# Kernel optimization log

Measured on AMD Instinct MI355X. Metric: run time of the kernel, lower is better.

The kernel has to match this reference:

```python
import jax, jax.numpy as jnp
import numpy as np

B, D, U = 4096, 1024, 1024  # batch, complex input dim, units


def _bias(u):
    # unit_forget_bias: zeros with forget-gate slice (i,f,c,o ordering) set to 1
    return jnp.zeros((4 * u,), jnp.float32).at[u:2 * u].set(1.0)


def setup_inputs() -> dict:
    key = jax.random.key(0)
    ks = jax.random.split(key, 7)
    s = 0.02  # kernel init scale
    return {
        "inputs": jax.random.normal(ks[0], (B, 2 * D), jnp.float32),
        "h_tm1": jax.random.normal(ks[1], (B, 2 * U), jnp.float32),
        "c_tm1": jax.random.normal(ks[2], (B, 2 * U), jnp.float32),
        "real_kernel": s * jax.random.normal(ks[3], (D, 4 * U), jnp.float32),
        "imaginary_kernel": s * jax.random.normal(ks[4], (D, 4 * U), jnp.float32),
        "real_recurrent_kernel": s * jax.random.normal(ks[5], (U, 4 * U), jnp.float32),
        "imaginary_recurrent_kernel": s * jax.random.normal(ks[6], (U, 4 * U), jnp.float32),
        "real_bias": _bias(U),
        "imaginary_bias": _bias(U),
    }


def hard_sigmoid(x):
    # keras hard_sigmoid: clip(0.2*x + 0.5, 0, 1)
    return jnp.clip(0.2 * x + 0.5, 0.0, 1.0)


def reference(inputs, h_tm1, c_tm1, real_kernel, imaginary_kernel,
              real_recurrent_kernel, imaginary_recurrent_kernel,
              real_bias, imaginary_bias):
    d = real_kernel.shape[0]
    u = real_recurrent_kernel.shape[0]
    xr, xi = inputs[:, :d], inputs[:, d:]          # [B,D] real/imag
    hr, hi = h_tm1[:, :u], h_tm1[:, u:]            # [B,U]
    # x @ [[R,-I],[I,R]] == [xr@R + xi@I, xi@R - xr@I]; done once over all 4 gates
    zr = xr @ real_kernel + xi @ imaginary_kernel \
         + hr @ real_recurrent_kernel + hi @ imaginary_recurrent_kernel + real_bias      # [B,4U]
    zi = xi @ real_kernel - xr @ imaginary_kernel \
         + hi @ real_recurrent_kernel - hr @ imaginary_recurrent_kernel + imaginary_bias  # [B,4U]

    def gate(g):  # concatenated real|imag pre-activation for gate g (i,f,c,o)
        s = slice(g * u, (g + 1) * u)
        return jnp.concatenate([zr[:, s], zi[:, s]], axis=-1)  # [B,2U]

    i = hard_sigmoid(gate(0))
    f = hard_sigmoid(gate(1))
    c = f * c_tm1 + i * jnp.tanh(gate(2))
    o = hard_sigmoid(gate(3))
    h = o * jnp.tanh(c)
    return h, c
```

## Files before the change

kernel.cpp:

```cpp
#include <hip/hip_runtime.h>

typedef unsigned short u16;
typedef unsigned int   u32;

typedef __bf16 bf16x8 __attribute__((ext_vector_type(8)));
typedef float  f32x4  __attribute__((ext_vector_type(4)));

typedef const __attribute__((address_space(1))) u32 GAS;
typedef __attribute__((address_space(3))) u32 LAS;

__device__ __forceinline__ u16 f2bf(float f) {
  u32 u = __builtin_bit_cast(u32, f);
  return (u16)((u + 0x7FFFu + ((u >> 16) & 1u)) >> 16);
}

__global__ __launch_bounds__(256) void build_x_k(
    const float* __restrict__ inp, const float* __restrict__ h,
    u16* __restrict__ X3) {
  __shared__ float t[64 * 65];
  const int tid = threadIdx.x;
  const int tx = tid & 15, ty = tid >> 4;
  const int m0 = blockIdx.y * 64, k0 = blockIdx.x * 64;
  const int sel = k0 >> 10;
  const int kc = k0 & 1023;
  const float* s1 = (sel == 0 || sel == 2 || sel == 4) ? inp : h;
  const int c1 = (sel == 2 || sel == 3) ? (1024 + kc) : kc;
  const bool pair = (sel >= 4);
#pragma unroll
  for (int rr = 0; rr < 4; ++rr) {
    const int m = rr * 16 + ty;
    float4 v = *(const float4*)&s1[(size_t)(m0 + m) * 2048 + c1 + tx * 4];
    if (pair) {
      const float4 w = *(const float4*)&s1[(size_t)(m0 + m) * 2048 + c1 + 1024 + tx * 4];
      v.x += w.x; v.y += w.y; v.z += w.z; v.w += w.w;
    }
    t[(tx * 4 + 0) * 65 + m] = v.x;
    t[(tx * 4 + 1) * 65 + m] = v.y;
    t[(tx * 4 + 2) * 65 + m] = v.z;
    t[(tx * 4 + 3) * 65 + m] = v.w;
  }
  __syncthreads();
#pragma unroll
  for (int rep = 0; rep < 2; ++rep) {
    const int cell = rep * 256 + tid;
    const int kblk = cell >> 6, m = cell & 63;
    union { u16 s[8]; uint4 v; } tmp;
#pragma unroll
    for (int i = 0; i < 8; ++i) tmp.s[i] = f2bf(t[(kblk * 8 + i) * 65 + m]);
    *(uint4*)&X3[((size_t)(k0 / 8 + kblk) * 4096 + m0 + m) * 8] = tmp.v;
  }
}

__global__ __launch_bounds__(256) void build_w_k(
    const float* __restrict__ Kr, const float* __restrict__ Ki,
    const float* __restrict__ Rr, const float* __restrict__ Ri,
    u16* __restrict__ W3) {
  __shared__ float t[4 * 1032];
  const int tid = threadIdx.x;
  const int tx = tid & 15, ty = tid >> 4;
  const int jhi = blockIdx.y;
  const int k0 = blockIdx.x * 64;
  const int sel = k0 >> 10;
  const int krow = k0 & 1023;
  const int jbase = jhi * 16;
  const float* sA = (sel == 0) ? Kr : (sel == 1) ? Rr : (sel == 2) ? Ki
                  : (sel == 3) ? Ri : (sel == 4) ? Kr : Rr;
  const float* sB = (sel == 4) ? Ki : (sel == 5) ? Ri : nullptr;
#pragma unroll
  for (int g = 0; g < 4; ++g) {
    const int cs = g * 1024 + jbase + tx;
#pragma unroll
    for (int rr = 0; rr < 4; ++rr) {
      const int k = rr * 16 + ty;
      float v = sA[(size_t)(krow + k) * 4096 + cs];
      if (sel >= 4) v -= sB[(size_t)(krow + k) * 4096 + cs];
      t[g * 1032 + k * 16 + tx] = v;
    }
  }
  __syncthreads();
#pragma unroll
  for (int rep = 0; rep < 2; ++rep) {
    const int cell = rep * 256 + tid;
    const int kblk = cell >> 6, n = cell & 63;
    const int g = n >> 4, jlo = n & 15;
    union { u16 s[8]; uint4 v; } tmp;
#pragma unroll
    for (int i = 0; i < 8; ++i)
      tmp.s[i] = f2bf(t[g * 1032 + (kblk * 8 + i) * 16 + jlo]);
    *(uint4*)&W3[((size_t)(k0 / 8 + kblk) * 4096 + (size_t)jhi * 64 + n) * 8] = tmp.v;
  }
}

#define KT 96

#define SLOT_BODY(ACC)                                                      \
  _Pragma("unroll")                                                         \
  for (int ks = 0; ks < 2; ++ks) {                                          \
    bf16x8 af[4], bfr[4];                                                   \
    _Pragma("unroll")                                                       \
    for (int mf = 0; mf < 4; ++mf)                                          \
      af[mf] = *(const bf16x8*)&buf[aoff + ks * 4096 + mf * 128];           \
    _Pragma("unroll")                                                       \
    for (int nf = 0; nf < 4; ++nf)                                          \
      bfr[nf] = *(const bf16x8*)&buf[boff + ks * 8192 + nf * 128];          \
    __builtin_amdgcn_s_setprio(1);                                          \
    _Pragma("unroll")                                                       \
    for (int mf = 0; mf < 4; ++mf)                                          \
      _Pragma("unroll")                                                     \
      for (int nf = 0; nf < 4; ++nf)                                        \
        ACC[mf][nf] = __builtin_amdgcn_mfma_f32_16x16x32_bf16(              \
            af[mf], bfr[nf], ACC[mf][nf], 0, 0, 0);                         \
    __builtin_amdgcn_s_setprio(0);                                          \
  }

__global__ __launch_bounds__(512, 2) void clstm_gemm_k(
    const u16* __restrict__ X3, const u16* __restrict__ W3,
    const float* __restrict__ cprev, const float* __restrict__ rb,
    const float* __restrict__ ib, float* __restrict__ out) {
  __shared__ __align__(16) u16 lds[3][24576];
  const int tid = threadIdx.x;
  const int lane = tid & 63, wave = tid >> 6;
  const int wr = wave >> 2, wc = wave & 3;
  const int orig = blockIdx.x;
  const int wg = (orig & 7) * 64 + (orig >> 3);
  const int mb = wg & 31, nb = wg >> 5;
  const int m0 = mb * 128, n0 = nb * 256;

  f32x4 a1[4][4] = {}, a2[4][4] = {};

  auto stage = [&](int t, int bi) {
    u16* buf = &lds[bi][0];
    const size_t kb0 = (size_t)t * 8;
#pragma unroll
    for (int i = 0; i < 6; ++i) {
      const int c = wave * 6 + i;
      if (c < 16) {
        const int kblk = c >> 1, half = c & 1;
        const u16* g = X3 + ((kb0 + kblk) * 4096 + (size_t)(m0 + half * 64 + lane)) * 8;
        __builtin_amdgcn_global_load_lds((GAS*)g, (LAS*)&buf[(kblk * 128 + half * 64) * 8],
                                         16, 0, 0);
      } else {
        const int cc = c - 16, kblk = cc >> 2, grp = cc & 3;
        const u16* g = W3 + ((kb0 + kblk) * 4096 + (size_t)(n0 + grp * 64 + lane)) * 8;
        __builtin_amdgcn_global_load_lds((GAS*)g,
                                         (LAS*)&buf[8192 + (kblk * 256 + grp * 64) * 8],
                                         16, 0, 0);
      }
    }
  };

  auto slot_sync = [&](int t, int stb) {
    if (t < KT - 1)
      asm volatile("s_waitcnt vmcnt(6)" ::: "memory");
    else
      asm volatile("s_waitcnt vmcnt(0)" ::: "memory");
    __builtin_amdgcn_s_barrier();
    __builtin_amdgcn_sched_barrier(0);
    if (t + 2 < KT) stage(t + 2, stb);
  };

  const int hi = lane >> 4, lo = lane & 15;
  const int aoff = (hi * 128 + wr * 64 + lo) * 8;
  const int boff = 8192 + (hi * 256 + wc * 64 + lo) * 8;

  stage(0, 0);
  stage(1, 1);
  int cb = 0;

  for (int t = 0; t < 32; ++t) {
    int stb = cb + 2; if (stb >= 3) stb -= 3;
    slot_sync(t, stb);
    const u16* buf = &lds[cb][0];
    SLOT_BODY(a1)
    ++cb; if (cb == 3) cb = 0;
  }
  for (int t = 32; t < 64; ++t) {
    int stb = cb + 2; if (stb >= 3) stb -= 3;
    slot_sync(t, stb);
    const u16* buf = &lds[cb][0];
    SLOT_BODY(a2)
    ++cb; if (cb == 3) cb = 0;
  }
#pragma unroll
  for (int mf = 0; mf < 4; ++mf)
#pragma unroll
    for (int nf = 0; nf < 4; ++nf) {
      const f32x4 t0 = a1[mf][nf];
      a1[mf][nf] = t0 + a2[mf][nf];
      a2[mf][nf] = a2[mf][nf] - t0;
    }
  for (int t = 64; t < KT; ++t) {
    int stb = cb + 2; if (stb >= 3) stb -= 3;
    slot_sync(t, stb);
    const u16* buf = &lds[cb][0];
    SLOT_BODY(a2)
    ++cb; if (cb == 3) cb = 0;
  }

  const int j = (nb * 4 + wc) * 16 + lo;
  float rbias[4], ibias[4];
#pragma unroll
  for (int g = 0; g < 4; ++g) {
    rbias[g] = rb[g * 1024 + j];
    ibias[g] = ib[g * 1024 + j];
  }
#pragma unroll
  for (int mf = 0; mf < 4; ++mf) {
    const int rowb = m0 + wr * 64 + mf * 16 + hi * 4;
#pragma unroll
    for (int r = 0; r < 4; ++r) {
      const size_t row = (size_t)(rowb + r);
      {
        const float z0 = a1[mf][0][r] + rbias[0];
        const float z1 = a1[mf][1][r] + rbias[1];
        const float z2 = a1[mf][2][r] + rbias[2];
        const float z3 = a1[mf][3][r] + rbias[3];
        const float ig = fminf(fmaxf(0.2f * z0 + 0.5f, 0.0f), 1.0f);
        const float fg = fminf(fmaxf(0.2f * z1 + 0.5f, 0.0f), 1.0f);
        const float og = fminf(fmaxf(0.2f * z3 + 0.5f, 0.0f), 1.0f);
        const float cp = cprev[row * 2048 + j];
        const float cn = fg * cp + ig * tanhf(z2);
        const float hn = og * tanhf(cn);
        out[row * 2048 + j] = hn;
        out[(size_t)8388608 + row * 2048 + j] = cn;
      }
      {
        const float z0 = a2[mf][0][r] + ibias[0];
        const float z1 = a2[mf][1][r] + ibias[1];
        const float z2 = a2[mf][2][r] + ibias[2];
        const float z3 = a2[mf][3][r] + ibias[3];
        const float ig = fminf(fmaxf(0.2f * z0 + 0.5f, 0.0f), 1.0f);
        const float fg = fminf(fmaxf(0.2f * z1 + 0.5f, 0.0f), 1.0f);
        const float og = fminf(fmaxf(0.2f * z3 + 0.5f, 0.0f), 1.0f);
        const float cp = cprev[row * 2048 + 1024 + j];
        const float cn = fg * cp + ig * tanhf(z2);
        const float hn = og * tanhf(cn);
        out[row * 2048 + 1024 + j] = hn;
        out[(size_t)8388608 + row * 2048 + 1024 + j] = cn;
      }
    }
  }
}

extern "C" void kernel_launch(void* const* d_in, const int* in_sizes, int n_in,
                              void* d_out, int out_size, void* d_ws, size_t ws_size,
                              hipStream_t stream) {
  const float* inputs = (const float*)d_in[0];
  const float* h_tm1  = (const float*)d_in[1];
  const float* c_tm1  = (const float*)d_in[2];
  const float* Kr     = (const float*)d_in[3];
  const float* Ki     = (const float*)d_in[4];
  const float* Rr     = (const float*)d_in[5];
  const float* Ri     = (const float*)d_in[6];
  const float* rb     = (const float*)d_in[7];
  const float* ib     = (const float*)d_in[8];
  float* out = (float*)d_out;

  u16* X3 = (u16*)d_ws;
  u16* W3 = X3 + (size_t)768 * 4096 * 8;

  build_x_k<<<dim3(96, 64), 256, 0, stream>>>(inputs, h_tm1, X3);
  build_w_k<<<dim3(96, 64), 256, 0, stream>>>(Kr, Ki, Rr, Ri, W3);
  clstm_gemm_k<<<dim3(512, 1), 512, 0, stream>>>(X3, W3, c_tm1, rb, ib, out);
}
```

Before: 294.6 us.

## Split each K-slot into two barrier-synced phases interleaving loads with MFMA

Restructures the main GEMM loop so each K tile runs as two phases. Each phase issues half of the next-next tile's global-to-LDS loads, waits on LDS reads, runs its MFMA block, and places barriers around it, in the style of a ping-pong schedule. The aim is to spread memory issue across the compute and keep the waves in lockstep so loads overlap better with matrix math. In exchange it doubles the barrier count per tile and adds waits that could stall the pipeline.

```diff
diff --git a/kernel.cpp b/kernel.cpp
--- a/kernel.cpp
+++ b/kernel.cpp
@@ -93,16 +93,25 @@
 
 #define KT 96
 
-#define SLOT_BODY(ACC)                                                      \
-  _Pragma("unroll")                                                         \
-  for (int ks = 0; ks < 2; ++ks) {                                          \
+#define PHASE(ACC, KS, HALF)                                                \
+  {                                                                         \
     bf16x8 af[4], bfr[4];                                                   \
     _Pragma("unroll")                                                       \
     for (int mf = 0; mf < 4; ++mf)                                          \
-      af[mf] = *(const bf16x8*)&buf[aoff + ks * 4096 + mf * 128];           \
+      af[mf] = *(const bf16x8*)&buf[aoff + (KS) * 4096 + mf * 128];         \
     _Pragma("unroll")                                                       \
     for (int nf = 0; nf < 4; ++nf)                                          \
-      bfr[nf] = *(const bf16x8*)&buf[boff + ks * 8192 + nf * 128];          \
+      bfr[nf] = *(const bf16x8*)&buf[boff + (KS) * 8192 + nf * 128];        \
+    if (t + 2 < KT) stage3(t + 2, stb, HALF);                               \
+    if (HALF) {                                                             \
+      if (t + 1 == KT - 1)                                                  \
+        asm volatile("s_waitcnt vmcnt(0)" ::: "memory");                    \
+      else if (t + 1 < KT - 1)                                              \
+        asm volatile("s_waitcnt vmcnt(6)" ::: "memory");                    \
+    }                                                                       \
+    __builtin_amdgcn_s_barrier();                                           \
+    asm volatile("s_waitcnt lgkmcnt(0)" ::: "memory");                      \
+    __builtin_amdgcn_sched_barrier(0);                                      \
     __builtin_amdgcn_s_setprio(1);                                          \
     _Pragma("unroll")                                                       \
     for (int mf = 0; mf < 4; ++mf)                                          \
@@ -111,6 +120,7 @@
         ACC[mf][nf] = __builtin_amdgcn_mfma_f32_16x16x32_bf16(              \
             af[mf], bfr[nf], ACC[mf][nf], 0, 0, 0);                         \
     __builtin_amdgcn_s_setprio(0);                                          \
+    __builtin_amdgcn_s_barrier();                                           \
   }
 
 __global__ __launch_bounds__(512, 2) void clstm_gemm_k(
@@ -128,16 +138,16 @@
 
   f32x4 a1[4][4] = {}, a2[4][4] = {};
 
-  auto stage = [&](int t, int bi) {
+  auto stage3 = [&](int t, int bi, int half) {
     u16* buf = &lds[bi][0];
     const size_t kb0 = (size_t)t * 8;
 #pragma unroll
-    for (int i = 0; i < 6; ++i) {
+    for (int i = half * 3; i < half * 3 + 3; ++i) {
       const int c = wave * 6 + i;
       if (c < 16) {
-        const int kblk = c >> 1, half = c & 1;
-        const u16* g = X3 + ((kb0 + kblk) * 4096 + (size_t)(m0 + half * 64 + lane)) * 8;
-        __builtin_amdgcn_global_load_lds((GAS*)g, (LAS*)&buf[(kblk * 128 + half * 64) * 8],
+        const int kblk = c >> 1, half2 = c & 1;
+        const u16* g = X3 + ((kb0 + kblk) * 4096 + (size_t)(m0 + half2 * 64 + lane)) * 8;
+        __builtin_amdgcn_global_load_lds((GAS*)g, (LAS*)&buf[(kblk * 128 + half2 * 64) * 8],
                                          16, 0, 0);
       } else {
         const int cc = c - 16, kblk = cc >> 2, grp = cc & 3;
@@ -149,36 +159,28 @@
     }
   };
 
-  auto slot_sync = [&](int t, int stb) {
-    if (t < KT - 1)
-      asm volatile("s_waitcnt vmcnt(6)" ::: "memory");
-    else
-      asm volatile("s_waitcnt vmcnt(0)" ::: "memory");
-    __builtin_amdgcn_s_barrier();
-    __builtin_amdgcn_sched_barrier(0);
-    if (t + 2 < KT) stage(t + 2, stb);
-  };
-
   const int hi = lane >> 4, lo = lane & 15;
   const int aoff = (hi * 128 + wr * 64 + lo) * 8;
   const int boff = 8192 + (hi * 256 + wc * 64 + lo) * 8;
 
-  stage(0, 0);
-  stage(1, 1);
+  stage3(0, 0, 0); stage3(0, 0, 1);
+  stage3(1, 1, 0); stage3(1, 1, 1);
+  asm volatile("s_waitcnt vmcnt(6)" ::: "memory");
+  __builtin_amdgcn_s_barrier();
   int cb = 0;
 
   for (int t = 0; t < 32; ++t) {
     int stb = cb + 2; if (stb >= 3) stb -= 3;
-    slot_sync(t, stb);
     const u16* buf = &lds[cb][0];
-    SLOT_BODY(a1)
+    PHASE(a1, 0, 0)
+    PHASE(a1, 1, 1)
     ++cb; if (cb == 3) cb = 0;
   }
   for (int t = 32; t < 64; ++t) {
     int stb = cb + 2; if (stb >= 3) stb -= 3;
-    slot_sync(t, stb);
     const u16* buf = &lds[cb][0];
-    SLOT_BODY(a2)
+    PHASE(a2, 0, 0)
+    PHASE(a2, 1, 1)
     ++cb; if (cb == 3) cb = 0;
   }
 #pragma unroll
@@ -191,9 +193,9 @@
     }
   for (int t = 64; t < KT; ++t) {
     int stb = cb + 2; if (stb >= 3) stb -= 3;
-    slot_sync(t, stb);
     const u16* buf = &lds[cb][0];
-    SLOT_BODY(a2)
+    PHASE(a2, 0, 0)
+    PHASE(a2, 1, 1)
     ++cb; if (cb == 3) cb = 0;
   }
 
```

After: 390.3 us. +32.5%, slower.
